# Kernel optimization log

Measured on AMD Instinct MI355X. Metric: run time of the kernel, lower is better.

## Reference

```python
import jax, jax.numpy as jnp
import numpy as np

N = 100000
E = 1600000
IN_C, HID, HEADS, OUT_C = 128, 32, 4, 32
NEG_SLOPE = 0.2


def gat_layer(x, edge_index, W, att_src, att_dst, bias, concat):
    """PyG-style GATConv: h = xW, per-edge attention, segment softmax over dst, scatter-add."""
    n = x.shape[0]
    H, C = att_src.shape
    h = (x @ W).reshape(n, H, C)                      # [N, H, C]
    src, dst = edge_index[0], edge_index[1]
    a_s = jnp.sum(h * att_src, axis=-1)               # [N, H]
    a_d = jnp.sum(h * att_dst, axis=-1)               # [N, H]
    e = jax.nn.leaky_relu(a_s[src] + a_d[dst], NEG_SLOPE)   # [E, H]
    # numerically stable segment softmax over incoming edges of each dst node
    m = jax.ops.segment_max(e, dst, num_segments=n)   # [N, H]
    ex = jnp.exp(e - m[dst])
    denom = jax.ops.segment_sum(ex, dst, num_segments=n)
    alpha = ex / denom[dst]                           # [E, H]
    msg = h[src] * alpha[:, :, None]                  # [E, H, C]
    out = jax.ops.segment_sum(msg, dst, num_segments=n)  # [N, H, C]
    out = out.reshape(n, H * C) if concat else out.mean(axis=1)
    return out + bias


def add_self_loops(edge_index, n):
    ar = jnp.arange(n, dtype=edge_index.dtype)
    loops = jnp.stack([ar, ar])
    return jnp.concatenate([edge_index, loops], axis=1)


def setup_inputs() -> dict:
    key = jax.random.key(0)
    ks = jax.random.split(key, 10)
    x = jax.random.normal(ks[0], (N, IN_C), dtype=jnp.float32)
    edge_index = jax.random.randint(ks[1], (2, E), 0, N, dtype=jnp.int64)
    s = 0.1
    W1 = jax.random.normal(ks[2], (IN_C, HEADS * HID), dtype=jnp.float32) * s
    att_src1 = jax.random.normal(ks[3], (HEADS, HID), dtype=jnp.float32) * s
    att_dst1 = jax.random.normal(ks[4], (HEADS, HID), dtype=jnp.float32) * s
    b1 = jnp.zeros((HEADS * HID,), dtype=jnp.float32)
    W2 = jax.random.normal(ks[5], (HEADS * HID, OUT_C), dtype=jnp.float32) * s
    att_src2 = jax.random.normal(ks[6], (1, OUT_C), dtype=jnp.float32) * s
    att_dst2 = jax.random.normal(ks[7], (1, OUT_C), dtype=jnp.float32) * s
    b2 = jnp.zeros((OUT_C,), dtype=jnp.float32)
    return {"x": x, "edge_index": edge_index,
            "W1": W1, "att_src1": att_src1, "att_dst1": att_dst1, "b1": b1,
            "W2": W2, "att_src2": att_src2, "att_dst2": att_dst2, "b2": b2}


def reference(x, edge_index, W1, att_src1, att_dst1, b1, W2, att_src2, att_dst2, b2):
    ei = add_self_loops(edge_index, x.shape[0])
    h = gat_layer(x, ei, W1, att_src1, att_dst1, b1, concat=True)
    h = jax.nn.elu(h)
    h = gat_layer(h, ei, W2, att_src2, att_dst2, b2, concat=False)
    return jax.nn.log_softmax(h, axis=1)
```

## Files before the change

kernel.cpp:

```cpp
#include <hip/hip_runtime.h>
#include <hip/hip_fp16.h>
#include <math.h>

#define IN_C   128
#define HEADS  4
#define F1     128
#define OUT_C  32
#define NEG    0.2f
#define SH     8
#define CHA    8192
#define SCB    4096

__device__ __forceinline__ unsigned short f2h(float f) {
    return __half_as_ushort(__float2half_rn(f));
}
__device__ __forceinline__ float h2f(unsigned short u) {
    return __half2float(__ushort_as_half(u));
}
__device__ __forceinline__ float hlo(unsigned u) { return h2f((unsigned short)(u & 0xffffu)); }
__device__ __forceinline__ float hhi(unsigned u) { return h2f((unsigned short)(u >> 16)); }
__device__ __forceinline__ unsigned pk2(float a, float b) {
    return (unsigned)f2h(a) | ((unsigned)f2h(b) << 16);
}
typedef _Float16 h2v __attribute__((ext_vector_type(2)));
__device__ __forceinline__ h2v u2h2(unsigned u) {
    h2v r; __builtin_memcpy(&r, &u, 4); return r;
}
__device__ __forceinline__ float dot2(unsigned a, unsigned b, float c) {
    return __builtin_amdgcn_fdot2(u2h2(a), u2h2(b), c, false);
}
#define PERM_LO 0x05040100u
#define PERM_HI 0x07060302u
__device__ __forceinline__ float pdot(unsigned b, unsigned a, unsigned sel, h2v pv, float c) {
    return __builtin_amdgcn_fdot2(u2h2(__builtin_amdgcn_perm(b, a, sel)), pv, c, false);
}

__global__ __launch_bounds__(256) void k_bhist(
    const int* __restrict__ ei, int* __restrict__ bmat, int E_, int n, int NB, int NC)
{
    __shared__ int h[512];
    int t = threadIdx.x, c = blockIdx.x;
    for (int i = t; i < NB; i += 256) h[i] = 0;
    __syncthreads();
    int e0 = c * CHA, e1 = min(e0 + CHA, E_ + n);
    for (int e = e0 + t; e < e1; e += 256) {
        int d = (e < E_) ? ei[E_ + e] : e - E_;
        atomicAdd(&h[d >> SH], 1);
    }
    __syncthreads();
    for (int i = t; i < NB; i += 256) bmat[i * NC + c] = h[i];
}

__global__ __launch_bounds__(256) void k_scanA(
    int* __restrict__ bmat, int* __restrict__ bsums, int M)
{
    __shared__ int sm[256];
    int t = threadIdx.x;
    int base = blockIdx.x * SCB + t * 16;
    int v[16];
    int s = 0;
    #pragma unroll
    for (int j = 0; j < 16; ++j) {
        int i = base + j;
        v[j] = (i < M) ? bmat[i] : 0;
        s += v[j];
    }
    sm[t] = s;
    __syncthreads();
    for (int off = 1; off < 256; off <<= 1) {
        int a = (t >= off) ? sm[t - off] : 0;
        __syncthreads();
        sm[t] += a;
        __syncthreads();
    }
    int excl = sm[t] - s;
    #pragma unroll
    for (int j = 0; j < 16; ++j) {
        int i = base + j;
        if (i < M) bmat[i] = excl;
        excl += v[j];
    }
    if (t == 255) bsums[blockIdx.x] = sm[255];
}

__global__ __launch_bounds__(256) void k_scanB(int* __restrict__ bsums, int NBLK)
{
    __shared__ int sm[256];
    int t = threadIdx.x;
    int v = (t < NBLK) ? bsums[t] : 0;
    sm[t] = v;
    __syncthreads();
    for (int off = 1; off < 256; off <<= 1) {
        int a = (t >= off) ? sm[t - off] : 0;
        __syncthreads();
        sm[t] += a;
        __syncthreads();
    }
    if (t < NBLK) bsums[t] = sm[t] - v;
}


__global__ __launch_bounds__(256) void k_bscatter(
    const int* __restrict__ ei, const int* __restrict__ bmat,
    const int* __restrict__ bsums, unsigned* __restrict__ recs,
    int E_, int n, int NB, int NC)
{
    __shared__ int cur[512];
    int t = threadIdx.x, c = blockIdx.x;
    for (int i = t; i < NB; i += 256) {
        int m = i * NC + c;
        cur[i] = bmat[m] + bsums[m >> 12];
    }
    __syncthreads();
    int e0 = c * CHA, e1 = min(e0 + CHA, E_ + n);
    for (int e = e0 + t; e < e1; e += 256) {
        int s, d;
        if (e < E_) { s = ei[e]; d = ei[E_ + e]; } else { s = d = e - E_; }
        int b = d >> SH;
        int p = atomicAdd(&cur[b], 1);
        recs[p] = ((unsigned)(d & ((1 << SH) - 1)) << 17) | (unsigned)s;
    }
}

__global__ __launch_bounds__(256) void k_bfill(
    const unsigned* __restrict__ recs, const int* __restrict__ bmat,
    const int* __restrict__ bsums, int* __restrict__ row_off,
    int* __restrict__ csr, int n, int NB, int NC, int EE)
{
    __shared__ int deg[256];
    __shared__ int cur[256];
    int t = threadIdx.x, b = blockIdx.x;
    int m0 = b * NC;
    int r0 = bmat[m0] + bsums[m0 >> 12];
    int r1 = EE;
    if (b + 1 < NB) {
        int m1 = (b + 1) * NC;
        r1 = bmat[m1] + bsums[m1 >> 12];
    }
    deg[t] = 0;
    __syncthreads();
    for (int i = r0 + t; i < r1; i += 256)
        atomicAdd(&deg[recs[i] >> 17], 1);
    __syncthreads();
    int v = deg[t];
    for (int off = 1; off < 256; off <<= 1) {
        int a = (t >= off) ? deg[t - off] : 0;
        __syncthreads();
        deg[t] += a;
        __syncthreads();
    }
    int excl = deg[t] - v;
    int dst = (b << SH) + t;
    if (dst < n) row_off[dst] = r0 + excl;
    cur[t] = excl;
    if (b == NB - 1 && t == 0) row_off[n] = EE;
    __syncthreads();
    for (int i = r0 + t; i < r1; i += 256) {
        unsigned rec = recs[i];
        int dl = rec >> 17;
        int p = atomicAdd(&cur[dl], 1);
        csr[r0 + p] = (int)(rec & 0x1FFFFu);
    }
}

__global__ __launch_bounds__(256) void k_gemm1(
    const float* __restrict__ x, const float* __restrict__ W,
    const float* __restrict__ as_w, const float* __restrict__ ad_w,
    unsigned short* __restrict__ h1h, float* __restrict__ as1,
    float* __restrict__ ad1, int n)
{
    __shared__ unsigned Ws2[64 * 64];
    __shared__ unsigned xs2[64 * 64];
    int t = threadIdx.x;
    int half = blockIdx.x & 1;
    int n0 = (blockIdx.x >> 1) * 64;

    for (int i = t; i < 64 * 16; i += 256) {
        int k2 = i >> 4, c4 = (i & 15) * 4;
        const float* w0 = &W[(2 * k2) * 128 + half * 64 + c4];
        const float* w1 = &W[(2 * k2 + 1) * 128 + half * 64 + c4];
        float4 a = *(const float4*)w0;
        float4 b = *(const float4*)w1;
        uint4 p;
        p.x = pk2(a.x, b.x); p.y = pk2(a.y, b.y);
        p.z = pk2(a.z, b.z); p.w = pk2(a.w, b.w);
        *(uint4*)&Ws2[k2 * 64 + c4] = p;
    }
    for (int i = t; i < 64 * 32; i += 256) {
        int nl = i & 63, k4 = (i >> 6) * 4;
        int nn = n0 + nl;
        float4 v = (nn < n) ? *(const float4*)&x[(size_t)nn * 128 + k4]
                            : make_float4(0.f, 0.f, 0.f, 0.f);
        xs2[(k4 >> 1) * 64 + nl]       = pk2(v.x, v.y);
        xs2[((k4 >> 1) + 1) * 64 + nl] = pk2(v.z, v.w);
    }
    __syncthreads();

    int tx = t & 15, ty = t >> 4;
    float acc[4][4] = {};
    #pragma unroll 4
    for (int k2 = 0; k2 < 64; ++k2) {
        uint4 a = *(uint4*)&xs2[k2 * 64 + ty * 4];
        uint4 b = *(uint4*)&Ws2[k2 * 64 + tx * 4];
        unsigned av[4] = {a.x, a.y, a.z, a.w};
        unsigned bv[4] = {b.x, b.y, b.z, b.w};
        #pragma unroll
        for (int i = 0; i < 4; ++i)
            #pragma unroll
            for (int j = 0; j < 4; ++j)
                acc[i][j] = dot2(av[i], bv[j], acc[i][j]);
    }
    int cbase = half * 64 + tx * 4;
    float4 aws = *(const float4*)&as_w[cbase];
    float4 awd = *(const float4*)&ad_w[cbase];
    float sa[4], sd[4];
    #pragma unroll
    for (int i = 0; i < 4; ++i) {
        int nn = n0 + ty * 4 + i;
        sa[i] = acc[i][0]*aws.x + acc[i][1]*aws.y + acc[i][2]*aws.z + acc[i][3]*aws.w;
        sd[i] = acc[i][0]*awd.x + acc[i][1]*awd.y + acc[i][2]*awd.z + acc[i][3]*awd.w;
        if (nn < n) {
            ushort4 p;
            p.x = f2h(acc[i][0]); p.y = f2h(acc[i][1]);
            p.z = f2h(acc[i][2]); p.w = f2h(acc[i][3]);
            *(ushort4*)&h1h[(size_t)nn * 128 + cbase] = p;
        }
    }
    #pragma unroll
    for (int o = 1; o < 8; o <<= 1) {
        #pragma unroll
        for (int i = 0; i < 4; ++i) {
            sa[i] += __shfl_xor(sa[i], o);
            sd[i] += __shfl_xor(sd[i], o);
        }
    }
    if ((tx & 7) == 0) {
        int head = half * 2 + (tx >> 3);
        #pragma unroll
        for (int i = 0; i < 4; ++i) {
            int nn = n0 + ty * 4 + i;
            if (nn < n) {
                as1[(size_t)nn * 4 + head] = sa[i];
                ad1[(size_t)nn * 4 + head] = sd[i];
            }
        }
    }
}

__global__ __launch_bounds__(256) void k_gat1(
    const int* __restrict__ row_off, const int* __restrict__ csr,
    const float* __restrict__ as1, const float* __restrict__ ad1,
    const unsigned short* __restrict__ h1h, const float* __restrict__ b1,
    const float* __restrict__ W2, const float* __restrict__ as2w,
    const float* __restrict__ ad2w, unsigned short* __restrict__ h2h,
    float* __restrict__ as2, float* __restrict__ ad2, int n)
{
    __shared__ int      s_src[16][36];
    __shared__ unsigned s_pw[16][4][17];
    __shared__ unsigned W2s[64 * 32];
    __shared__ unsigned zs[16][66];
    int t = threadIdx.x;

    for (int i = t; i < 64 * 8; i += 256) {
        int k2 = i >> 3, c4 = (i & 7) * 4;
        float4 a = *(const float4*)&W2[(2 * k2) * 32 + c4];
        float4 b = *(const float4*)&W2[(2 * k2 + 1) * 32 + c4];
        uint4 p;
        p.x = pk2(a.x, b.x); p.y = pk2(a.y, b.y);
        p.z = pk2(a.z, b.z); p.w = pk2(a.w, b.w);
        *(uint4*)&W2s[k2 * 32 + c4] = p;
    }
    __syncthreads();

    int nb = t >> 4;
    int hl = t & 15;
    int node = blockIdx.x * 16 + nb;
    if (node < n) {
        int* ssrc = s_src[nb];
        unsigned (*spw)[17] = s_pw[nb];

        const char* h1b = (const char*)h1h;
        int chb  = hl << 4;
        int head = hl >> 2;

        float4 addv = *(const float4*)&ad1[(size_t)node * 4];
        int beg = row_off[node], end = row_off[node + 1];

        float sr0 = 0.f, sr1 = 0.f, sr2 = 0.f, sr3 = 0.f;
        float acc0 = 0.f, acc1 = 0.f, acc2 = 0.f, acc3 = 0.f;
        float acc4 = 0.f, acc5 = 0.f, acc6 = 0.f, acc7 = 0.f;

        for (int c = beg; c < end; c += 32) {
            int cnt = min(32, end - c);
            int e0 = hl << 1;
            float ls0 = 0.f, ls1 = 0.f, ls2 = 0.f, ls3 = 0.f;
            if (e0 < cnt) {
                int sA = csr[c + e0];
                ssrc[e0] = sA << 8;
                float4 avA = *(const float4*)(as1 + ((unsigned)sA << 2));
                float v;
                unsigned short qa0, qa1, qa2, qa3;
                unsigned short qb0 = 0, qb1 = 0, qb2 = 0, qb3 = 0;
                v = avA.x + addv.x; v = v > 0.f ? v : NEG * v; qa0 = f2h(__expf(fminf(v, 10.f)));
                v = avA.y + addv.y; v = v > 0.f ? v : NEG * v; qa1 = f2h(__expf(fminf(v, 10.f)));
                v = avA.z + addv.z; v = v > 0.f ? v : NEG * v; qa2 = f2h(__expf(fminf(v, 10.f)));
                v = avA.w + addv.w; v = v > 0.f ? v : NEG * v; qa3 = f2h(__expf(fminf(v, 10.f)));
                if (e0 + 1 < cnt) {
                    int sB = csr[c + e0 + 1];
                    ssrc[e0 + 1] = sB << 8;
                    float4 avB = *(const float4*)(as1 + ((unsigned)sB << 2));
                    v = avB.x + addv.x; v = v > 0.f ? v : NEG * v; qb0 = f2h(__expf(fminf(v, 10.f)));
                    v = avB.y + addv.y; v = v > 0.f ? v : NEG * v; qb1 = f2h(__expf(fminf(v, 10.f)));
                    v = avB.z + addv.z; v = v > 0.f ? v : NEG * v; qb2 = f2h(__expf(fminf(v, 10.f)));
                    v = avB.w + addv.w; v = v > 0.f ? v : NEG * v; qb3 = f2h(__expf(fminf(v, 10.f)));
                }
                spw[0][hl] = (unsigned)qa0 | ((unsigned)qb0 << 16);
                spw[1][hl] = (unsigned)qa1 | ((unsigned)qb1 << 16);
                spw[2][hl] = (unsigned)qa2 | ((unsigned)qb2 << 16);
                spw[3][hl] = (unsigned)qa3 | ((unsigned)qb3 << 16);
                ls0 = h2f(qa0) + h2f(qb0);
                ls1 = h2f(qa1) + h2f(qb1);
                ls2 = h2f(qa2) + h2f(qb2);
                ls3 = h2f(qa3) + h2f(qb3);
            }
            #pragma unroll
            for (int o = 8; o; o >>= 1) {
                ls0 += __shfl_xor(ls0, o);
                ls1 += __shfl_xor(ls1, o);
                ls2 += __shfl_xor(ls2, o);
                ls3 += __shfl_xor(ls3, o);
            }
            sr0 += ls0; sr1 += ls1; sr2 += ls2; sr3 += ls3;
            __threadfence_block();

            #define MAC8(A, B, pw) {                                          \
                h2v pv = u2h2(pw);                                            \
                acc0 = pdot(B.x, A.x, PERM_LO, pv, acc0);                     \
                acc1 = pdot(B.x, A.x, PERM_HI, pv, acc1);                     \
                acc2 = pdot(B.y, A.y, PERM_LO, pv, acc2);                     \
                acc3 = pdot(B.y, A.y, PERM_HI, pv, acc3);                     \
                acc4 = pdot(B.z, A.z, PERM_LO, pv, acc4);                     \
                acc5 = pdot(B.z, A.z, PERM_HI, pv, acc5);                     \
                acc6 = pdot(B.w, A.w, PERM_LO, pv, acc6);                     \
                acc7 = pdot(B.w, A.w, PERM_HI, pv, acc7);                     \
            }
            int j = 0;
            for (; j + 8 <= cnt; j += 8) {
                int2 o0 = *(const int2*)&ssrc[j];
                int2 o1 = *(const int2*)&ssrc[j + 2];
                int2 o2 = *(const int2*)&ssrc[j + 4];
                int2 o3 = *(const int2*)&ssrc[j + 6];
                int w0 = j >> 1;
                unsigned pw0 = spw[head][w0];
                unsigned pw1 = spw[head][w0 + 1];
                unsigned pw2 = spw[head][w0 + 2];
                unsigned pw3 = spw[head][w0 + 3];
                uint4 A0 = *(const uint4*)(h1b + (unsigned)(o0.x + chb));
                uint4 B0 = *(const uint4*)(h1b + (unsigned)(o0.y + chb));
                uint4 A1 = *(const uint4*)(h1b + (unsigned)(o1.x + chb));
                uint4 B1 = *(const uint4*)(h1b + (unsigned)(o1.y + chb));
                uint4 A2 = *(const uint4*)(h1b + (unsigned)(o2.x + chb));
                uint4 B2 = *(const uint4*)(h1b + (unsigned)(o2.y + chb));
                uint4 A3 = *(const uint4*)(h1b + (unsigned)(o3.x + chb));
                uint4 B3 = *(const uint4*)(h1b + (unsigned)(o3.y + chb));
                MAC8(A0, B0, pw0);
                MAC8(A1, B1, pw1);
                MAC8(A2, B2, pw2);
                MAC8(A3, B3, pw3);
            }
            for (; j + 2 <= cnt; j += 2) {
                int2 oo = *(const int2*)&ssrc[j];
                unsigned pw = spw[head][j >> 1];
                uint4 A = *(const uint4*)(h1b + (unsigned)(oo.x + chb));
                uint4 B = *(const uint4*)(h1b + (unsigned)(oo.y + chb));
                MAC8(A, B, pw);
            }
            if (j < cnt) {
                int o0 = ssrc[j];
                float p = hlo(spw[head][j >> 1]);
                uint4 A = *(const uint4*)(h1b + (unsigned)(o0 + chb));
                acc0 = fmaf(p, hlo(A.x), acc0);
                acc1 = fmaf(p, hhi(A.x), acc1);
                acc2 = fmaf(p, hlo(A.y), acc2);
                acc3 = fmaf(p, hhi(A.y), acc3);
                acc4 = fmaf(p, hlo(A.z), acc4);
                acc5 = fmaf(p, hhi(A.z), acc5);
                acc6 = fmaf(p, hlo(A.w), acc6);
                acc7 = fmaf(p, hhi(A.w), acc7);
            }
            #undef MAC8
        }
        float srh = head == 0 ? sr0 : head == 1 ? sr1 : head == 2 ? sr2 : sr3;
        float inv = 1.0f / srh;
        float4 bb0 = *(const float4*)&b1[hl * 8];
        float4 bb1 = *(const float4*)&b1[hl * 8 + 4];
        float v0 = acc0 * inv + bb0.x;
        float v1 = acc1 * inv + bb0.y;
        float v2 = acc2 * inv + bb0.z;
        float v3 = acc3 * inv + bb0.w;
        float v4 = acc4 * inv + bb1.x;
        float v5 = acc5 * inv + bb1.y;
        float v6 = acc6 * inv + bb1.z;
        float v7 = acc7 * inv + bb1.w;
        v0 = v0 > 0.f ? v0 : (__expf(v0) - 1.f);
        v1 = v1 > 0.f ? v1 : (__expf(v1) - 1.f);
        v2 = v2 > 0.f ? v2 : (__expf(v2) - 1.f);
        v3 = v3 > 0.f ? v3 : (__expf(v3) - 1.f);
        v4 = v4 > 0.f ? v4 : (__expf(v4) - 1.f);
        v5 = v5 > 0.f ? v5 : (__expf(v5) - 1.f);
        v6 = v6 > 0.f ? v6 : (__expf(v6) - 1.f);
        v7 = v7 > 0.f ? v7 : (__expf(v7) - 1.f);

        unsigned* zrow = zs[nb];
        zrow[hl * 4 + 0] = pk2(v0, v1);
        zrow[hl * 4 + 1] = pk2(v2, v3);
        zrow[hl * 4 + 2] = pk2(v4, v5);
        zrow[hl * 4 + 3] = pk2(v6, v7);
        __threadfence_block();
        int c0 = hl * 2;
        float a0 = 0.f, a1 = 0.f;
        #pragma unroll 8
        for (int k2 = 0; k2 < 64; ++k2) {
            unsigned zp = zrow[k2];
            uint2 wp = *(const uint2*)&W2s[k2 * 32 + c0];
            a0 = dot2(zp, wp.x, a0);
            a1 = dot2(zp, wp.y, a1);
        }
        *(unsigned*)&h2h[(size_t)node * 32 + c0] = pk2(a0, a1);
        float2 asw = *(const float2*)&as2w[c0];
        float2 adw = *(const float2*)&ad2w[c0];
        float sa = a0 * asw.x + a1 * asw.y;
        float sd = a0 * adw.x + a1 * adw.y;
        #pragma unroll
        for (int o = 8; o; o >>= 1) {
            sa += __shfl_xor(sa, o);
            sd += __shfl_xor(sd, o);
        }
        if (hl == 0) { as2[node] = sa; ad2[node] = sd; }
    }
}

__global__ __launch_bounds__(256) void k_gat2(
    const int* __restrict__ row_off, const int* __restrict__ csr,
    const float* __restrict__ as2, const float* __restrict__ ad2,
    const unsigned short* __restrict__ h2h, const float* __restrict__ b2,
    float* __restrict__ y, int n)
{
    int nb = threadIdx.x >> 2;
    int hl = threadIdx.x & 3;
    int node = blockIdx.x * 64 + nb;
    if (node >= n) return;
    __shared__ int            s_src[64][34];
    __shared__ unsigned short s_p16[64][34];
    int* ssrc = s_src[nb];
    unsigned short* sp16 = s_p16[nb];

    const char* h2b = (const char*)h2h;
    int chb = hl << 4;

    float addv = ad2[node];
    int beg = row_off[node], end = row_off[node + 1];
    float sr = 0.f;
    float acc0 = 0.f, acc1 = 0.f, acc2 = 0.f, acc3 = 0.f;
    float acc4 = 0.f, acc5 = 0.f, acc6 = 0.f, acc7 = 0.f;

    for (int c = beg; c < end; c += 32) {
        int cnt = min(32, end - c);
        int e0 = hl << 3;
        float ls = 0.f;
        #pragma unroll
        for (int k = 0; k < 8; k += 2) {
            int e = e0 + k;
            if (e < cnt) {
                unsigned short qa, qb = 0;
                int sA = csr[c + e];
                ssrc[e] = sA << 6;
                float v = as2[(unsigned)sA] + addv;
                v = v > 0.f ? v : NEG * v;
                qa = f2h(__expf(fminf(v, 10.f)));
                if (e + 1 < cnt) {
                    int sB = csr[c + e + 1];
                    ssrc[e + 1] = sB << 6;
                    float w2 = as2[(unsigned)sB] + addv;
                    w2 = w2 > 0.f ? w2 : NEG * w2;
                    qb = f2h(__expf(fminf(w2, 10.f)));
                }
                *(unsigned*)&sp16[e] = (unsigned)qa | ((unsigned)qb << 16);
                ls += h2f(qa) + h2f(qb);
            }
        }
        ls += __shfl_xor(ls, 1);
        ls += __shfl_xor(ls, 2);
        sr += ls;
        __threadfence_block();

        #define PAIR2(j) {                                                    \
            int2 oo = *(const int2*)&ssrc[j];                                 \
            unsigned pp = *(const unsigned*)&sp16[j];                         \
            uint4 A = *(const uint4*)(h2b + (unsigned)(oo.x + chb));          \
            uint4 B = *(const uint4*)(h2b + (unsigned)(oo.y + chb));          \
            h2v pv = u2h2(pp);                                                \
            acc0 = pdot(B.x, A.x, PERM_LO, pv, acc0);                         \
            acc1 = pdot(B.x, A.x, PERM_HI, pv, acc1);                         \
            acc2 = pdot(B.y, A.y, PERM_LO, pv, acc2);                         \
            acc3 = pdot(B.y, A.y, PERM_HI, pv, acc3);                         \
            acc4 = pdot(B.z, A.z, PERM_LO, pv, acc4);                         \
            acc5 = pdot(B.z, A.z, PERM_HI, pv, acc5);                         \
            acc6 = pdot(B.w, A.w, PERM_LO, pv, acc6);                         \
            acc7 = pdot(B.w, A.w, PERM_HI, pv, acc7);                         \
        }
        int jj = 0;
        for (; jj + 4 <= cnt; jj += 4) {
            PAIR2(jj);
            PAIR2(jj + 2);
        }
        if (jj + 2 <= cnt) {
            PAIR2(jj);
            jj += 2;
        }
        if (jj < cnt) {
            int o0 = ssrc[jj];
            float p = h2f(sp16[jj]);
            uint4 A = *(const uint4*)(h2b + (unsigned)(o0 + chb));
            acc0 = fmaf(p, hlo(A.x), acc0);
            acc1 = fmaf(p, hhi(A.x), acc1);
            acc2 = fmaf(p, hlo(A.y), acc2);
            acc3 = fmaf(p, hhi(A.y), acc3);
            acc4 = fmaf(p, hlo(A.z), acc4);
            acc5 = fmaf(p, hhi(A.z), acc5);
            acc6 = fmaf(p, hlo(A.w), acc6);
            acc7 = fmaf(p, hhi(A.w), acc7);
        }
        #undef PAIR2
    }
    float inv = 1.0f / sr;
    float4 bb0 = *(const float4*)&b2[hl * 8];
    float4 bb1 = *(const float4*)&b2[hl * 8 + 4];
    float v0 = acc0 * inv + bb0.x;
    float v1 = acc1 * inv + bb0.y;
    float v2 = acc2 * inv + bb0.z;
    float v3 = acc3 * inv + bb0.w;
    float v4 = acc4 * inv + bb1.x;
    float v5 = acc5 * inv + bb1.y;
    float v6 = acc6 * inv + bb1.z;
    float v7 = acc7 * inv + bb1.w;
    float m = fmaxf(fmaxf(fmaxf(v0, v1), fmaxf(v2, v3)),
                    fmaxf(fmaxf(v4, v5), fmaxf(v6, v7)));
    m = fmaxf(m, __shfl_xor(m, 1));
    m = fmaxf(m, __shfl_xor(m, 2));
    float ss = __expf(v0 - m) + __expf(v1 - m) + __expf(v2 - m) + __expf(v3 - m)
             + __expf(v4 - m) + __expf(v5 - m) + __expf(v6 - m) + __expf(v7 - m);
    ss += __shfl_xor(ss, 1);
    ss += __shfl_xor(ss, 2);
    float lg = m + logf(ss);
    float* yr = &y[(size_t)node * OUT_C + hl * 8];
    *(float4*)yr       = make_float4(v0 - lg, v1 - lg, v2 - lg, v3 - lg);
    *(float4*)(yr + 4) = make_float4(v4 - lg, v5 - lg, v6 - lg, v7 - lg);
}

extern "C" void kernel_launch(void* const* d_in, const int* in_sizes, int n_in,
                              void* d_out, int out_size, void* d_ws, size_t ws_size,
                              hipStream_t stream) {
    const float* x    = (const float*)d_in[0];
    const int*   ei   = (const int*)d_in[1];
    const float* W1   = (const float*)d_in[2];
    const float* as1w = (const float*)d_in[3];
    const float* ad1w = (const float*)d_in[4];
    const float* b1   = (const float*)d_in[5];
    const float* W2   = (const float*)d_in[6];
    const float* as2w = (const float*)d_in[7];
    const float* ad2w = (const float*)d_in[8];
    const float* b2   = (const float*)d_in[9];
    float* out = (float*)d_out;

    int n  = in_sizes[0] / IN_C;
    int E_ = in_sizes[1] / 2;
    int EE = E_ + n;

    int NB = (n + (1 << SH) - 1) >> SH;
    int NC = (EE + CHA - 1) / CHA;
    int M  = NB * NC;
    int NBLK = (M + SCB - 1) / SCB;

    char* w = (char*)d_ws;
    size_t off = 0;
    auto take = [&](size_t elems) { void* p = w + off; off += ((elems * 4 + 255) & ~(size_t)255); return p; };
    int* bmat      = (int*)take((size_t)M);
    int* bsums     = (int*)take(256);
    unsigned* recs = (unsigned*)take((size_t)EE);
    int* row_off   = (int*)take((size_t)n + 1);
    int* csr       = (int*)take((size_t)EE);
    float* as1     = (float*)take((size_t)n * 4);
    float* ad1     = (float*)take((size_t)n * 4);
    unsigned short* h1h = (unsigned short*)take((size_t)n * 64);
    unsigned short* h2h = (unsigned short*)take((size_t)n * 16);
    float* as2     = (float*)take((size_t)n);
    float* ad2     = (float*)take((size_t)n);

    k_bhist   <<<NC, 256, 0, stream>>>(ei, bmat, E_, n, NB, NC);
    k_scanA   <<<NBLK, 256, 0, stream>>>(bmat, bsums, M);
    k_scanB   <<<1, 256, 0, stream>>>(bsums, NBLK);
    k_bscatter<<<NC, 256, 0, stream>>>(ei, bmat, bsums, recs, E_, n, NB, NC);
    k_bfill   <<<NB, 256, 0, stream>>>(recs, bmat, bsums, row_off, csr, n, NB, NC, EE);

    int nt = (n + 63) / 64;
    k_gemm1<<<nt * 2, 256, 0, stream>>>(x, W1, as1w, ad1w, h1h, as1, ad1, n);

    int gG = (n + 15) / 16;
    k_gat1<<<gG, 256, 0, stream>>>(row_off, csr, as1, ad1, h1h, b1,
                                   W2, as2w, ad2w, h2h, as2, ad2, n);

    int gG2 = (n + 63) / 64;
    k_gat2<<<gG2, 256, 0, stream>>>(row_off, csr, as2, ad2, h2h, b2, out, n);
}
```

Before: 302.2 us.

## Fuse bucket histogram into GEMM launch and inline block-sum scan

Merges the destination-bucket histogram kernel into the first GEMM kernel as extra leading blocks, so the histogram and the feature transform run concurrently in one launch. It also removes the single-block scanB kernel: bscatter and bfill now each recompute the exclusive prefix of the block sums with a warp shuffle scan. This saves two launches and the serial gaps between them. The cost is redundant tiny scans in every block, and the inline scan only handles up to 32 block sums.

```diff
diff --git a/kernel.cpp b/kernel.cpp
--- a/kernel.cpp
+++ b/kernel.cpp
@@ -35,145 +35,35 @@
     return __builtin_amdgcn_fdot2(u2h2(__builtin_amdgcn_perm(b, a, sel)), pv, c, false);
 }
 
-__global__ __launch_bounds__(256) void k_bhist(
-    const int* __restrict__ ei, int* __restrict__ bmat, int E_, int n, int NB, int NC)
-{
-    __shared__ int h[512];
-    int t = threadIdx.x, c = blockIdx.x;
-    for (int i = t; i < NB; i += 256) h[i] = 0;
-    __syncthreads();
-    int e0 = c * CHA, e1 = min(e0 + CHA, E_ + n);
-    for (int e = e0 + t; e < e1; e += 256) {
-        int d = (e < E_) ? ei[E_ + e] : e - E_;
-        atomicAdd(&h[d >> SH], 1);
-    }
-    __syncthreads();
-    for (int i = t; i < NB; i += 256) bmat[i * NC + c] = h[i];
-}
-
-__global__ __launch_bounds__(256) void k_scanA(
-    int* __restrict__ bmat, int* __restrict__ bsums, int M)
-{
-    __shared__ int sm[256];
-    int t = threadIdx.x;
-    int base = blockIdx.x * SCB + t * 16;
-    int v[16];
-    int s = 0;
-    #pragma unroll
-    for (int j = 0; j < 16; ++j) {
-        int i = base + j;
-        v[j] = (i < M) ? bmat[i] : 0;
-        s += v[j];
-    }
-    sm[t] = s;
-    __syncthreads();
-    for (int off = 1; off < 256; off <<= 1) {
-        int a = (t >= off) ? sm[t - off] : 0;
-        __syncthreads();
-        sm[t] += a;
-        __syncthreads();
-    }
-    int excl = sm[t] - s;
-    #pragma unroll
-    for (int j = 0; j < 16; ++j) {
-        int i = base + j;
-        if (i < M) bmat[i] = excl;
-        excl += v[j];
-    }
-    if (t == 255) bsums[blockIdx.x] = sm[255];
-}
-
-__global__ __launch_bounds__(256) void k_scanB(int* __restrict__ bsums, int NBLK)
-{
-    __shared__ int sm[256];
-    int t = threadIdx.x;
-    int v = (t < NBLK) ? bsums[t] : 0;
-    sm[t] = v;
-    __syncthreads();
-    for (int off = 1; off < 256; off <<= 1) {
-        int a = (t >= off) ? sm[t - off] : 0;
-        __syncthreads();
-        sm[t] += a;
-        __syncthreads();
-    }
-    if (t < NBLK) bsums[t] = sm[t] - v;
-}
-
-
-__global__ __launch_bounds__(256) void k_bscatter(
-    const int* __restrict__ ei, const int* __restrict__ bmat,
-    const int* __restrict__ bsums, unsigned* __restrict__ recs,
-    int E_, int n, int NB, int NC)
-{
-    __shared__ int cur[512];
-    int t = threadIdx.x, c = blockIdx.x;
-    for (int i = t; i < NB; i += 256) {
-        int m = i * NC + c;
-        cur[i] = bmat[m] + bsums[m >> 12];
-    }
-    __syncthreads();
-    int e0 = c * CHA, e1 = min(e0 + CHA, E_ + n);
-    for (int e = e0 + t; e < e1; e += 256) {
-        int s, d;
-        if (e < E_) { s = ei[e]; d = ei[E_ + e]; } else { s = d = e - E_; }
-        int b = d >> SH;
-        int p = atomicAdd(&cur[b], 1);
-        recs[p] = ((unsigned)(d & ((1 << SH) - 1)) << 17) | (unsigned)s;
-    }
-}
-
-__global__ __launch_bounds__(256) void k_bfill(
-    const unsigned* __restrict__ recs, const int* __restrict__ bmat,
-    const int* __restrict__ bsums, int* __restrict__ row_off,
-    int* __restrict__ csr, int n, int NB, int NC, int EE)
-{
-    __shared__ int deg[256];
-    __shared__ int cur[256];
-    int t = threadIdx.x, b = blockIdx.x;
-    int m0 = b * NC;
-    int r0 = bmat[m0] + bsums[m0 >> 12];
-    int r1 = EE;
-    if (b + 1 < NB) {
-        int m1 = (b + 1) * NC;
-        r1 = bmat[m1] + bsums[m1 >> 12];
-    }
-    deg[t] = 0;
-    __syncthreads();
-    for (int i = r0 + t; i < r1; i += 256)
-        atomicAdd(&deg[recs[i] >> 17], 1);
-    __syncthreads();
-    int v = deg[t];
-    for (int off = 1; off < 256; off <<= 1) {
-        int a = (t >= off) ? deg[t - off] : 0;
-        __syncthreads();
-        deg[t] += a;
-        __syncthreads();
-    }
-    int excl = deg[t] - v;
-    int dst = (b << SH) + t;
-    if (dst < n) row_off[dst] = r0 + excl;
-    cur[t] = excl;
-    if (b == NB - 1 && t == 0) row_off[n] = EE;
-    __syncthreads();
-    for (int i = r0 + t; i < r1; i += 256) {
-        unsigned rec = recs[i];
-        int dl = rec >> 17;
-        int p = atomicAdd(&cur[dl], 1);
-        csr[r0 + p] = (int)(rec & 0x1FFFFu);
-    }
-}
-
-__global__ __launch_bounds__(256) void k_gemm1(
+__global__ __launch_bounds__(256) void k_gemm1b(
     const float* __restrict__ x, const float* __restrict__ W,
     const float* __restrict__ as_w, const float* __restrict__ ad_w,
+    const int* __restrict__ ei, int* __restrict__ bmat,
     unsigned short* __restrict__ h1h, float* __restrict__ as1,
-    float* __restrict__ ad1, int n)
+    float* __restrict__ ad1, int n, int E_, int NB, int NC)
 {
     __shared__ unsigned Ws2[64 * 64];
     __shared__ unsigned xs2[64 * 64];
     int t = threadIdx.x;
-    int half = blockIdx.x & 1;
-    int n0 = (blockIdx.x >> 1) * 64;
+
+    if ((int)blockIdx.x < NC) {
+        int* h = (int*)Ws2;
+        int c = blockIdx.x;
+        for (int i = t; i < NB; i += 256) h[i] = 0;
+        __syncthreads();
+        int e0 = c * CHA, e1 = min(e0 + CHA, E_ + n);
+        for (int e = e0 + t; e < e1; e += 256) {
+            int d = (e < E_) ? ei[E_ + e] : e - E_;
+            atomicAdd(&h[d >> SH], 1);
+        }
+        __syncthreads();
+        for (int i = t; i < NB; i += 256) bmat[i * NC + c] = h[i];
+        return;
+    }
+
+    int gb = (int)blockIdx.x - NC;
+    int half = gb & 1;
+    int n0 = (gb >> 1) * 64;
 
     for (int i = t; i < 64 * 16; i += 256) {
         int k2 = i >> 4, c4 = (i & 15) * 4;
@@ -244,6 +134,124 @@
                 ad1[(size_t)nn * 4 + head] = sd[i];
             }
         }
+    }
+}
+
+__global__ __launch_bounds__(256) void k_scanA(
+    int* __restrict__ bmat, int* __restrict__ bsums, int M)
+{
+    __shared__ int sm[256];
+    int t = threadIdx.x;
+    int base = blockIdx.x * SCB + t * 16;
+    int v[16];
+    int s = 0;
+    #pragma unroll
+    for (int j = 0; j < 16; ++j) {
+        int i = base + j;
+        v[j] = (i < M) ? bmat[i] : 0;
+        s += v[j];
+    }
+    sm[t] = s;
+    __syncthreads();
+    for (int off = 1; off < 256; off <<= 1) {
+        int a = (t >= off) ? sm[t - off] : 0;
+        __syncthreads();
+        sm[t] += a;
+        __syncthreads();
+    }
+    int excl = sm[t] - s;
+    #pragma unroll
+    for (int j = 0; j < 16; ++j) {
+        int i = base + j;
+        if (i < M) bmat[i] = excl;
+        excl += v[j];
+    }
+    if (t == 255) bsums[blockIdx.x] = sm[255];
+}
+
+__global__ __launch_bounds__(256) void k_bscatter(
+    const int* __restrict__ ei, const int* __restrict__ bmat,
+    const int* __restrict__ bsums, unsigned* __restrict__ recs,
+    int E_, int n, int NB, int NC, int NBLK)
+{
+    __shared__ int cur[512];
+    __shared__ int pref[32];
+    int t = threadIdx.x, c = blockIdx.x;
+    if (t < 32) {
+        int v0 = (t < NBLK) ? bsums[t] : 0;
+        int v = v0;
+        #pragma unroll
+        for (int o = 1; o < 32; o <<= 1) {
+            int u = __shfl_up(v, o);
+            if (t >= o) v += u;
+        }
+        pref[t] = v - v0;
+    }
+    __syncthreads();
+    for (int i = t; i < NB; i += 256) {
+        int m = i * NC + c;
+        cur[i] = bmat[m] + pref[m >> 12];
+    }
+    __syncthreads();
+    int e0 = c * CHA, e1 = min(e0 + CHA, E_ + n);
+    for (int e = e0 + t; e < e1; e += 256) {
+        int s, d;
+        if (e < E_) { s = ei[e]; d = ei[E_ + e]; } else { s = d = e - E_; }
+        int b = d >> SH;
+        int p = atomicAdd(&cur[b], 1);
+        recs[p] = ((unsigned)(d & ((1 << SH) - 1)) << 17) | (unsigned)s;
+    }
+}
+
+__global__ __launch_bounds__(256) void k_bfill(
+    const unsigned* __restrict__ recs, const int* __restrict__ bmat,
+    const int* __restrict__ bsums, int* __restrict__ row_off,
+    int* __restrict__ csr, int n, int NB, int NC, int EE, int NBLK)
+{
+    __shared__ int deg[256];
+    __shared__ int cur[256];
+    __shared__ int pref[32];
+    int t = threadIdx.x, b = blockIdx.x;
+    if (t < 32) {
+        int v0 = (t < NBLK) ? bsums[t] : 0;
+        int v = v0;
+        #pragma unroll
+        for (int o = 1; o < 32; o <<= 1) {
+            int u = __shfl_up(v, o);
+            if (t >= o) v += u;
+        }
+        pref[t] = v - v0;
+    }
+    deg[t] = 0;
+    __syncthreads();
+    int m0 = b * NC;
+    int r0 = bmat[m0] + pref[m0 >> 12];
+    int r1 = EE;
+    if (b + 1 < NB) {
+        int m1 = (b + 1) * NC;
+        r1 = bmat[m1] + pref[m1 >> 12];
+    }
+    for (int i = r0 + t; i < r1; i += 256)
+        atomicAdd(&deg[recs[i] >> 17], 1);
+    __syncthreads();
+    int v = deg[t];
+    for (int off = 1; off < 256; off <<= 1) {
+        int a = (t >= off) ? deg[t - off] : 0;
+        __syncthreads();
+        deg[t] += a;
+        __syncthreads();
+    }
+    int excl = deg[t] - v;
+    int dst = (b << SH) + t;
+    if (dst < n) row_off[dst] = r0 + excl;
+    cur[t] = excl;
+    if (b == NB - 1 && t == 0) row_off[n] = EE;
+    __syncthreads();
+    for (int i = r0 + t; i < r1; i += 256) {
+        unsigned rec = recs[i];
+        int dl = rec >> 17;
+        int p = atomicAdd(&cur[dl], 1);
+        csr[r0 + p] = (int)(rec & 0x1FFFFu);
     }
 }
 
@@ -597,14 +605,13 @@
     float* as2     = (float*)take((size_t)n);
     float* ad2     = (float*)take((size_t)n);
 
-    k_bhist   <<<NC, 256, 0, stream>>>(ei, bmat, E_, n, NB, NC);
+    int nt2 = 2 * ((n + 63) / 64);
+    k_gemm1b<<<NC + nt2, 256, 0, stream>>>(x, W1, as1w, ad1w, ei, bmat,
+                                           h1h, as1, ad1, n, E_, NB, NC);
+
     k_scanA   <<<NBLK, 256, 0, stream>>>(bmat, bsums, M);
-    k_scanB   <<<1, 256, 0, stream>>>(bsums, NBLK);
-    k_bscatter<<<NC, 256, 0, stream>>>(ei, bmat, bsums, recs, E_, n, NB, NC);
-    k_bfill   <<<NB, 256, 0, stream>>>(recs, bmat, bsums, row_off, csr, n, NB, NC, EE);
-
-    int nt = (n + 63) / 64;
-    k_gemm1<<<nt * 2, 256, 0, stream>>>(x, W1, as1w, ad1w, h1h, as1, ad1, n);
+    k_bscatter<<<NC, 256, 0, stream>>>(ei, bmat, bsums, recs, E_, n, NB, NC, NBLK);
+    k_bfill   <<<NB, 256, 0, stream>>>(recs, bmat, bsums, row_off, csr, n, NB, NC, EE, NBLK);
 
     int gG = (n + 15) / 16;
     k_gat1<<<gG, 256, 0, stream>>>(row_off, csr, as1, ad1, h1h, b1,
```

Measured after the change: 292.5 us. 1.03x faster.
